# Optimization experiments

Measured on AMD Instinct MI355X. Metric: run time of the kernel, lower is better.

The kernel has to match this reference:

```python
import jax, jax.numpy as jnp
import numpy as np

B, T, C = 1, 2_000_000, 16
NAN_FRAC = 0.05  # fraction of entries replaced by NaN, as the layer is a NaN-interpolation op


def setup_inputs() -> dict:
    key = jax.random.key(0)
    k_x, k_m = jax.random.split(key)
    x = jax.random.normal(k_x, (B, T, C), dtype=jnp.float32)
    nan_mask = jax.random.uniform(k_m, (B, T, C)) < NAN_FRAC
    x = jnp.where(nan_mask, jnp.float32(jnp.nan), x)
    return {"inputs": x}


def reference(inputs):
    # Vectorized form of the per-column loop: for each column, compute the
    # mean of the valid (non-NaN) entries along time and fill NaNs with it.
    # (Original code computes this per column with tf.reduce_mean + tf.map_fn
    # + tf.where/tf.fill; here it is a single fused pass.)
    mask = jnp.isnan(inputs)                       # [B, T, C]
    safe = jnp.where(mask, jnp.float32(0.0), inputs)
    valid = jnp.sum(jnp.logical_not(mask).astype(inputs.dtype), axis=1)  # [B, C]
    mean = jnp.sum(safe, axis=1) / jnp.maximum(valid, 1.0)               # [B, C]
    out = jnp.where(mask, mean[:, None, :], safe)  # broadcast NaN fill
    return out
```

## Files before the change

kernel.cpp:

```cpp
#include <hip/hip_runtime.h>

#define C_COLS 16
#define NT 256
#define NB1 1024
#define NB2 2048

__global__ __launch_bounds__(NT) void k_reduce(const float4* __restrict__ x4,
                                               long long n4,
                                               float* __restrict__ partials) {
    const int tid = threadIdx.x;
    const long long gid = (long long)blockIdx.x * NT + tid;
    const long long stride = (long long)gridDim.x * NT;

    float s0 = 0.f, s1 = 0.f, s2 = 0.f, s3 = 0.f;
    float c0 = 0.f, c1 = 0.f, c2 = 0.f, c3 = 0.f;

#define ACC(v)                                                              \
    do {                                                                    \
        bool m0 = ((v).x == (v).x); s0 += m0 ? (v).x : 0.f; c0 += m0 ? 1.f : 0.f; \
        bool m1 = ((v).y == (v).y); s1 += m1 ? (v).y : 0.f; c1 += m1 ? 1.f : 0.f; \
        bool m2 = ((v).z == (v).z); s2 += m2 ? (v).z : 0.f; c2 += m2 ? 1.f : 0.f; \
        bool m3 = ((v).w == (v).w); s3 += m3 ? (v).w : 0.f; c3 += m3 ? 1.f : 0.f; \
    } while (0)

    long long i = gid;
    for (; i + 7 * stride < n4; i += 8 * stride) {
        float4 va = x4[i];
        float4 vb = x4[i + stride];
        float4 vc = x4[i + 2 * stride];
        float4 vd = x4[i + 3 * stride];
        float4 ve = x4[i + 4 * stride];
        float4 vf = x4[i + 5 * stride];
        float4 vg = x4[i + 6 * stride];
        float4 vh = x4[i + 7 * stride];
        ACC(va); ACC(vb); ACC(vc); ACC(vd);
        ACC(ve); ACC(vf); ACC(vg); ACC(vh);
    }
    {
        float4 t0, t1, t2, t3, t4, t5, t6;
        bool h0 = (i + 0 * stride) < n4;
        bool h1 = (i + 1 * stride) < n4;
        bool h2 = (i + 2 * stride) < n4;
        bool h3 = (i + 3 * stride) < n4;
        bool h4 = (i + 4 * stride) < n4;
        bool h5 = (i + 5 * stride) < n4;
        bool h6 = (i + 6 * stride) < n4;
        if (h0) t0 = x4[i + 0 * stride];
        if (h1) t1 = x4[i + 1 * stride];
        if (h2) t2 = x4[i + 2 * stride];
        if (h3) t3 = x4[i + 3 * stride];
        if (h4) t4 = x4[i + 4 * stride];
        if (h5) t5 = x4[i + 5 * stride];
        if (h6) t6 = x4[i + 6 * stride];
        if (h0) ACC(t0);
        if (h1) ACC(t1);
        if (h2) ACC(t2);
        if (h3) ACC(t3);
        if (h4) ACC(t4);
        if (h5) ACC(t5);
        if (h6) ACC(t6);
    }
#undef ACC

    for (int off = 4; off < 64; off <<= 1) {
        s0 += __shfl_xor(s0, off, 64);
        s1 += __shfl_xor(s1, off, 64);
        s2 += __shfl_xor(s2, off, 64);
        s3 += __shfl_xor(s3, off, 64);
        c0 += __shfl_xor(c0, off, 64);
        c1 += __shfl_xor(c1, off, 64);
        c2 += __shfl_xor(c2, off, 64);
        c3 += __shfl_xor(c3, off, 64);
    }

    __shared__ float bsum[C_COLS];
    __shared__ float bcnt[C_COLS];
    if (tid < C_COLS) { bsum[tid] = 0.f; bcnt[tid] = 0.f; }
    __syncthreads();

    if ((tid & 63) < 4) {
        const int cb4 = (tid & 3) * 4;
        atomicAdd(&bsum[cb4 + 0], s0);
        atomicAdd(&bsum[cb4 + 1], s1);
        atomicAdd(&bsum[cb4 + 2], s2);
        atomicAdd(&bsum[cb4 + 3], s3);
        atomicAdd(&bcnt[cb4 + 0], c0);
        atomicAdd(&bcnt[cb4 + 1], c1);
        atomicAdd(&bcnt[cb4 + 2], c2);
        atomicAdd(&bcnt[cb4 + 3], c3);
    }
    __syncthreads();

    if (tid < C_COLS) {
        partials[(long long)blockIdx.x * 32 + tid] = bsum[tid];
        partials[(long long)blockIdx.x * 32 + C_COLS + tid] = bcnt[tid];
    }
}

__global__ __launch_bounds__(NT) void k_fill(const float4* __restrict__ x4,
                                             float4* __restrict__ o4,
                                             long long n4, long long n,
                                             const float* __restrict__ partials,
                                             int nb1) {
    const int tid = threadIdx.x;
    const long long gid = (long long)blockIdx.x * NT + tid;
    const long long stride = (long long)gridDim.x * NT;

    float4 pa, pb, pc, pd;
    const bool ha = (gid + 0 * stride) < n4;
    const bool hb = (gid + 1 * stride) < n4;
    const bool hc = (gid + 2 * stride) < n4;
    const bool hd = (gid + 3 * stride) < n4;
    if (ha) pa = x4[gid + 0 * stride];
    if (hb) pb = x4[gid + 1 * stride];
    if (hc) pc = x4[gid + 2 * stride];
    if (hd) pd = x4[gid + 3 * stride];

    __shared__ float ssum[NT];
    __shared__ float scnt[NT];
    __shared__ float smean[C_COLS];
    {
        const int c = tid & 15;
        const int r0 = tid >> 4;
        float S = 0.f, Cn = 0.f;
        #pragma unroll 8
        for (int p = r0; p < nb1; p += 16) {
            S  += partials[(long long)p * 32 + c];
            Cn += partials[(long long)p * 32 + 16 + c];
        }
        ssum[tid] = S;
        scnt[tid] = Cn;
        __syncthreads();
        if (tid < 16) {
            float SS = 0.f, CC = 0.f;
            for (int r = 0; r < 16; ++r) {
                SS += ssum[r * 16 + tid];
                CC += scnt[r * 16 + tid];
            }
            const float* x = (const float*)x4;
            for (long long j = n4 * 4; j < n; ++j) {
                if ((int)(j % 16) == tid) {
                    float v = x[j];
                    if (v == v) { SS += v; CC += 1.f; }
                }
            }
            smean[tid] = SS / fmaxf(CC, 1.f);
        }
        __syncthreads();
    }

    const int cb = (int)(gid & 3) * 4;
    const float m0 = smean[cb + 0];
    const float m1 = smean[cb + 1];
    const float m2 = smean[cb + 2];
    const float m3 = smean[cb + 3];

#define FIX_ST(v, idx)                                                      \
    do {                                                                    \
        float4 nv;                                                          \
        nv.x = ((v).x == (v).x) ? (v).x : m0;                               \
        nv.y = ((v).y == (v).y) ? (v).y : m1;                               \
        nv.z = ((v).z == (v).z) ? (v).z : m2;                               \
        nv.w = ((v).w == (v).w) ? (v).w : m3;                               \
        o4[idx] = nv;                                                       \
    } while (0)

    if (ha) FIX_ST(pa, gid + 0 * stride);
    if (hb) FIX_ST(pb, gid + 1 * stride);
    if (hc) FIX_ST(pc, gid + 2 * stride);
    if (hd) FIX_ST(pd, gid + 3 * stride);

    long long i = gid + 4 * stride;
    for (; i + 3 * stride < n4; i += 4 * stride) {
        float4 va = x4[i];
        float4 vb = x4[i + stride];
        float4 vc = x4[i + 2 * stride];
        float4 vd = x4[i + 3 * stride];
        FIX_ST(va, i);
        FIX_ST(vb, i + stride);
        FIX_ST(vc, i + 2 * stride);
        FIX_ST(vd, i + 3 * stride);
    }
    for (; i < n4; i += stride) {
        float4 v = x4[i];
        FIX_ST(v, i);
    }
#undef FIX_ST

    if (gid == 0) {
        const float* x = (const float*)x4;
        float* o = (float*)o4;
        for (long long j = n4 * 4; j < n; ++j) {
            float v = x[j];
            o[j] = (v == v) ? v : smean[(int)(j % 16)];
        }
    }
}

extern "C" void kernel_launch(void* const* d_in, const int* in_sizes, int n_in,
                              void* d_out, int out_size, void* d_ws, size_t ws_size,
                              hipStream_t stream) {
    const float* x = (const float*)d_in[0];
    float* out = (float*)d_out;
    const long long n = (long long)in_sizes[0];
    const long long n4 = n / 4;

    int nb1 = NB1;
    {
        long long cap = (long long)(ws_size / 4) / 32;
        if (cap < 1) cap = 1;
        if (nb1 > cap) nb1 = (int)cap;
    }
    float* partials = (float*)d_ws;

    k_reduce<<<nb1, NT, 0, stream>>>((const float4*)x, n4, partials);
    k_fill<<<NB2, NT, 0, stream>>>((const float4*)x, (float4*)out, n4, n,
                                   partials, nb1);
}
```

Measured before the change: 245.6 us.

## Fuse copy into reduction pass and patch NaN positions via per-block index lists

The reduction kernel now also copies the input straight to the output. It records the flat indices of NaN entries in a per-block shared-memory list, built with wave ballots and atomics, and writes that list to the workspace. A small patch kernel then computes the column means and scatters them only to the recorded positions. This removes the second full read of the input done by the old fill pass, at the cost of ballot and atomic work per element, 32 KB of LDS per block, and a workspace requirement. Each block list is capped at 8192 entries, so blocks with many more NaNs would silently be left unfilled; the old path remains as a fallback when the workspace is too small.

After: 281.3 us. 14.5% more time.

```diff
diff --git a/kernel.cpp b/kernel.cpp
--- a/kernel.cpp
+++ b/kernel.cpp
@@ -4,13 +4,24 @@
 #define NT 256
 #define NB1 1024
 #define NB2 2048
-
+#define SEG 8192
+
+template <int MODE>
 __global__ __launch_bounds__(NT) void k_reduce(const float4* __restrict__ x4,
+                                               float4* __restrict__ o4,
                                                long long n4,
-                                               float* __restrict__ partials) {
+                                               float* __restrict__ partials,
+                                               int* __restrict__ counts,
+                                               int* __restrict__ idx_g) {
     const int tid = threadIdx.x;
+    const int lane = tid & 63;
     const long long gid = (long long)blockIdx.x * NT + tid;
     const long long stride = (long long)gridDim.x * NT;
+
+    __shared__ int l_idx[MODE ? SEG : 1];
+    __shared__ int l_cnt;
+    if (MODE && tid == 0) l_cnt = 0;
+    if (MODE) __syncthreads();
 
     float s0 = 0.f, s1 = 0.f, s2 = 0.f, s3 = 0.f;
     float c0 = 0.f, c1 = 0.f, c2 = 0.f, c3 = 0.f;
@@ -21,6 +32,31 @@
         bool m1 = ((v).y == (v).y); s1 += m1 ? (v).y : 0.f; c1 += m1 ? 1.f : 0.f; \
         bool m2 = ((v).z == (v).z); s2 += m2 ? (v).z : 0.f; c2 += m2 ? 1.f : 0.f; \
         bool m3 = ((v).w == (v).w); s3 += m3 ? (v).w : 0.f; c3 += m3 ? 1.f : 0.f; \
+    } while (0)
+
+#define COLLECT1(pred, fidx)                                                \
+    do {                                                                    \
+        unsigned long long mm = __ballot(pred);                             \
+        int pc = (int)__popcll(mm);                                         \
+        int base = 0;                                                       \
+        if (lane == 0) base = atomicAdd(&l_cnt, pc);                        \
+        base = __shfl(base, 0, 64);                                         \
+        if (pred) {                                                         \
+            int pos = base + (int)__popcll(mm & ((1ull << lane) - 1ull));   \
+            if (pos < SEG) l_idx[pos] = (int)(fidx);                        \
+        }                                                                   \
+    } while (0)
+
+#define COPYCOLLECT(v, i)                                                   \
+    do {                                                                    \
+        if (MODE) {                                                         \
+            o4[(i)] = (v);                                                  \
+            long long fb = (i) * 4;                                         \
+            COLLECT1(!((v).x == (v).x), fb + 0);                            \
+            COLLECT1(!((v).y == (v).y), fb + 1);                            \
+            COLLECT1(!((v).z == (v).z), fb + 2);                            \
+            COLLECT1(!((v).w == (v).w), fb + 3);                            \
+        }                                                                   \
     } while (0)
 
     long long i = gid;
@@ -35,6 +71,14 @@
         float4 vh = x4[i + 7 * stride];
         ACC(va); ACC(vb); ACC(vc); ACC(vd);
         ACC(ve); ACC(vf); ACC(vg); ACC(vh);
+        COPYCOLLECT(va, i);
+        COPYCOLLECT(vb, i + stride);
+        COPYCOLLECT(vc, i + 2 * stride);
+        COPYCOLLECT(vd, i + 3 * stride);
+        COPYCOLLECT(ve, i + 4 * stride);
+        COPYCOLLECT(vf, i + 5 * stride);
+        COPYCOLLECT(vg, i + 6 * stride);
+        COPYCOLLECT(vh, i + 7 * stride);
     }
     {
         float4 t0, t1, t2, t3, t4, t5, t6;
@@ -59,7 +103,26 @@
         if (h4) ACC(t4);
         if (h5) ACC(t5);
         if (h6) ACC(t6);
-    }
+#define TAILCC(h, t, ii)                                                    \
+        if (MODE && (h)) {                                                  \
+            o4[(ii)] = (t);                                                 \
+            long long fb = (ii) * 4;                                        \
+            if (!((t).x == (t).x)) { int p = atomicAdd(&l_cnt, 1); if (p < SEG) l_idx[p] = (int)(fb + 0); } \
+            if (!((t).y == (t).y)) { int p = atomicAdd(&l_cnt, 1); if (p < SEG) l_idx[p] = (int)(fb + 1); } \
+            if (!((t).z == (t).z)) { int p = atomicAdd(&l_cnt, 1); if (p < SEG) l_idx[p] = (int)(fb + 2); } \
+            if (!((t).w == (t).w)) { int p = atomicAdd(&l_cnt, 1); if (p < SEG) l_idx[p] = (int)(fb + 3); } \
+        }
+        TAILCC(h0, t0, i + 0 * stride)
+        TAILCC(h1, t1, i + 1 * stride)
+        TAILCC(h2, t2, i + 2 * stride)
+        TAILCC(h3, t3, i + 3 * stride)
+        TAILCC(h4, t4, i + 4 * stride)
+        TAILCC(h5, t5, i + 5 * stride)
+        TAILCC(h6, t6, i + 6 * stride)
+#undef TAILCC
+    }
+#undef COPYCOLLECT
+#undef COLLECT1
 #undef ACC
 
     for (int off = 4; off < 64; off <<= 1) {
@@ -95,6 +158,70 @@
         partials[(long long)blockIdx.x * 32 + tid] = bsum[tid];
         partials[(long long)blockIdx.x * 32 + C_COLS + tid] = bcnt[tid];
     }
+
+    if (MODE) {
+        int cnt = l_cnt;
+        if (cnt > SEG) cnt = SEG;
+        if (tid == 0) counts[blockIdx.x] = cnt;
+        for (int k = tid; k < cnt; k += NT)
+            idx_g[(long long)blockIdx.x * SEG + k] = l_idx[k];
+    }
+}
+
+__global__ __launch_bounds__(NT) void k_patch(const float* __restrict__ partials,
+                                              int nb1,
+                                              const float* __restrict__ x,
+                                              long long n4, long long n,
+                                              float* __restrict__ out,
+                                              const int* __restrict__ counts,
+                                              const int* __restrict__ idx_g) {
+    const int tid = threadIdx.x;
+
+    __shared__ float ssum[NT];
+    __shared__ float scnt[NT];
+    __shared__ float smean[C_COLS];
+    {
+        const int c = tid & 15;
+        const int r0 = tid >> 4;
+        float S = 0.f, Cn = 0.f;
+        #pragma unroll 8
+        for (int p = r0; p < nb1; p += 16) {
+            S  += partials[(long long)p * 32 + c];
+            Cn += partials[(long long)p * 32 + 16 + c];
+        }
+        ssum[tid] = S;
+        scnt[tid] = Cn;
+        __syncthreads();
+        if (tid < 16) {
+            float SS = 0.f, CC = 0.f;
+            for (int r = 0; r < 16; ++r) {
+                SS += ssum[r * 16 + tid];
+                CC += scnt[r * 16 + tid];
+            }
+            for (long long j = n4 * 4; j < n; ++j) {
+                if ((int)(j % 16) == tid) {
+                    float v = x[j];
+                    if (v == v) { SS += v; CC += 1.f; }
+                }
+            }
+            smean[tid] = SS / fmaxf(CC, 1.f);
+        }
+        __syncthreads();
+    }
+
+    const int cnt = counts[blockIdx.x];
+    const int* seg = idx_g + (long long)blockIdx.x * SEG;
+    for (int k = tid; k < cnt; k += NT) {
+        int fidx = seg[k];
+        out[fidx] = smean[fidx & 15];
+    }
+
+    if (blockIdx.x == 0 && tid == 0) {
+        for (long long j = n4 * 4; j < n; ++j) {
+            float v = x[j];
+            out[j] = (v == v) ? v : smean[(int)(j % 16)];
+        }
+    }
 }
 
 __global__ __launch_bounds__(NT) void k_fill(const float4* __restrict__ x4,
@@ -105,16 +232,6 @@
     const int tid = threadIdx.x;
     const long long gid = (long long)blockIdx.x * NT + tid;
     const long long stride = (long long)gridDim.x * NT;
-
-    float4 pa, pb, pc, pd;
-    const bool ha = (gid + 0 * stride) < n4;
-    const bool hb = (gid + 1 * stride) < n4;
-    const bool hc = (gid + 2 * stride) < n4;
-    const bool hd = (gid + 3 * stride) < n4;
-    if (ha) pa = x4[gid + 0 * stride];
-    if (hb) pb = x4[gid + 1 * stride];
-    if (hc) pc = x4[gid + 2 * stride];
-    if (hd) pd = x4[gid + 3 * stride];
 
     __shared__ float ssum[NT];
     __shared__ float scnt[NT];
@@ -155,37 +272,15 @@
     const float m2 = smean[cb + 2];
     const float m3 = smean[cb + 3];
 
-#define FIX_ST(v, idx)                                                      \
-    do {                                                                    \
-        float4 nv;                                                          \
-        nv.x = ((v).x == (v).x) ? (v).x : m0;                               \
-        nv.y = ((v).y == (v).y) ? (v).y : m1;                               \
-        nv.z = ((v).z == (v).z) ? (v).z : m2;                               \
-        nv.w = ((v).w == (v).w) ? (v).w : m3;                               \
-        o4[idx] = nv;                                                       \
-    } while (0)
-
-    if (ha) FIX_ST(pa, gid + 0 * stride);
-    if (hb) FIX_ST(pb, gid + 1 * stride);
-    if (hc) FIX_ST(pc, gid + 2 * stride);
-    if (hd) FIX_ST(pd, gid + 3 * stride);
-
-    long long i = gid + 4 * stride;
-    for (; i + 3 * stride < n4; i += 4 * stride) {
-        float4 va = x4[i];
-        float4 vb = x4[i + stride];
-        float4 vc = x4[i + 2 * stride];
-        float4 vd = x4[i + 3 * stride];
-        FIX_ST(va, i);
-        FIX_ST(vb, i + stride);
-        FIX_ST(vc, i + 2 * stride);
-        FIX_ST(vd, i + 3 * stride);
-    }
-    for (; i < n4; i += stride) {
+    for (long long i = gid; i < n4; i += stride) {
         float4 v = x4[i];
-        FIX_ST(v, i);
-    }
-#undef FIX_ST
+        float4 nv;
+        nv.x = (v.x == v.x) ? v.x : m0;
+        nv.y = (v.y == v.y) ? v.y : m1;
+        nv.z = (v.z == v.z) ? v.z : m2;
+        nv.w = (v.w == v.w) ? v.w : m3;
+        o4[i] = nv;
+    }
 
     if (gid == 0) {
         const float* x = (const float*)x4;
@@ -205,15 +300,23 @@
     const long long n = (long long)in_sizes[0];
     const long long n4 = n / 4;
 
-    int nb1 = NB1;
-    {
+    const size_t need = (size_t)NB1 * 32 * 4 + (size_t)NB1 * 4 + (size_t)NB1 * SEG * 4;
+    float* partials = (float*)d_ws;
+    int* counts = (int*)((char*)d_ws + (size_t)NB1 * 32 * 4);
+    int* idx_g = (int*)((char*)counts + (size_t)NB1 * 4);
+
+    if (ws_size >= need) {
+        k_reduce<1><<<NB1, NT, 0, stream>>>((const float4*)x, (float4*)out, n4,
+                                            partials, counts, idx_g);
+        k_patch<<<NB1, NT, 0, stream>>>(partials, NB1, x, n4, n, out, counts, idx_g);
+    } else {
+        int nb1 = NB1;
         long long cap = (long long)(ws_size / 4) / 32;
         if (cap < 1) cap = 1;
         if (nb1 > cap) nb1 = (int)cap;
-    }
-    float* partials = (float*)d_ws;
-
-    k_reduce<<<nb1, NT, 0, stream>>>((const float4*)x, n4, partials);
-    k_fill<<<NB2, NT, 0, stream>>>((const float4*)x, (float4*)out, n4, n,
-                                   partials, nb1);
+        k_reduce<0><<<nb1, NT, 0, stream>>>((const float4*)x, (float4*)out, n4,
+                                            partials, nullptr, nullptr);
+        k_fill<<<NB2, NT, 0, stream>>>((const float4*)x, (float4*)out, n4, n,
+                                       partials, nb1);
+    }
 }
```
